# Kernel optimization log

Measured on AMD Instinct MI355X. Metric: run time of the kernel, lower is better.

The kernel has to match this reference:

```python
import jax, jax.numpy as jnp
import numpy as np


def _rope(xh, theta_factor):
    # xh: [H, S, Dqk]; rotate first half against second half (as in source)
    S, D = xh.shape[-2], xh.shape[-1]
    d_rope = D // 2
    rate = theta_factor * (-jnp.arange(0, d_rope, dtype=xh.dtype) / d_rope)
    pos = jnp.arange(0, S, dtype=xh.dtype)
    rot = pos[:, None] * rate[None, :]            # [S, d_rope]
    sin, cos = jnp.sin(rot), jnp.cos(rot)
    x1, x2 = xh[..., :d_rope], xh[..., d_rope:]
    y1 = cos * x1 - sin * x2
    y2 = sin * x1 + cos * x2
    return jnp.concatenate([y1, y2], axis=-1)


def _mha(x, y, q, k, v, o, theta_factor):
    S = x.shape[0]
    d_model = x.shape[1]
    x_scale = 1.0 / jnp.sqrt(jnp.array(x.shape[1], x.dtype))
    y_scale = 1.0 / jnp.sqrt(jnp.array(y.shape[1], x.dtype))
    # causal additive mask: 0 on/below diagonal, -1e9 above
    mask = (jnp.tril(jnp.ones((S, S), x.dtype)) - 1.0) * 1000000000.0
    # per-head projections (note: source uses x_scale for both q and k)
    pre_q = jnp.einsum('sd,hdk->hsk', x, q) * x_scale
    pre_k = jnp.einsum('td,hdk->htk', y, k) * x_scale
    vs = jnp.einsum('td,hdv->htv', y, v) * y_scale
    rq = _rope(pre_q, theta_factor)
    rk = _rope(pre_k, theta_factor)
    attn_scale = 1.0 / jnp.sqrt(jnp.array(rq.shape[-1], x.dtype))
    scores = jnp.einsum('hsk,htk->hst', rq, rk) * attn_scale + mask
    w = jax.nn.softmax(scores, axis=-1)           # [H, S, S]
    z = jnp.einsum('hst,htv->hsv', w, vs)         # [H, S, Dv]
    out_scale = 1.0 / jnp.sqrt(jnp.array(o.shape[0] * o.shape[1], x.dtype))
    return jnp.einsum('hsv,hvd->sd', z, o) * out_scale


def setup_inputs() -> dict:
    key = jax.random.key(0)
    ks = jax.random.split(key, 5)
    S, D, H, Dqk, Dv = 2048, 2048, 16, 128, 128
    return {
        'x': jax.random.normal(ks[0], (S, D), jnp.float32),
        'q': jax.random.normal(ks[1], (H, D, Dqk), jnp.float32),
        'k': jax.random.normal(ks[2], (H, D, Dqk), jnp.float32),
        'v': jax.random.normal(ks[3], (H, D, Dv), jnp.float32),
        'o': jax.random.normal(ks[4], (H, Dv, D), jnp.float32),
        'theta_factor': jnp.array(10000.0, jnp.float32),
    }


def reference(x, q, k, v, o, theta_factor):
    # self-attention path (y = x), scale = 1
    return _mha(x, x, q, k, v, o, theta_factor)
```

## Files before the change

### kernel.cpp

```cpp
#include <hip/hip_runtime.h>


#define S_LEN   2048
#define D_MODEL 2048
#define NHEAD   16
#define DHEAD   128

using f32x4   = __attribute__((ext_vector_type(4))) float;
using f32x16  = __attribute__((ext_vector_type(16))) float;
using bf16x8  = __attribute__((ext_vector_type(8))) __bf16;

__device__ __forceinline__ unsigned short f2bf(float f) {
  unsigned int u = __builtin_bit_cast(unsigned int, f);
  u += 0x7fffu + ((u >> 16) & 1u);
  return (unsigned short)(u >> 16);
}
__device__ __forceinline__ int chunks_of(int qt) { return (4 * qt + 13) / 10; }

__device__ __forceinline__ void gl_lds16(const unsigned short* g, char* l) {
  __builtin_amdgcn_global_load_lds(
      (const __attribute__((address_space(1))) unsigned int*)g,
      (__attribute__((address_space(3))) unsigned int*)l, 16, 0, 0);
}

__global__ void k_cvt(const float* __restrict__ in, unsigned short* __restrict__ out) {
  int i = (blockIdx.x * 256 + threadIdx.x) * 4;
  float4 v = *reinterpret_cast<const float4*>(in + i);
  ushort4 o; o.x = f2bf(v.x); o.y = f2bf(v.y); o.z = f2bf(v.z); o.w = f2bf(v.w);
  *reinterpret_cast<ushort4*>(out + i) = o;
}

__global__ void k_tab(const float* __restrict__ theta_p, float* __restrict__ sint,
                      float* __restrict__ cost) {
  int i = blockIdx.x * 256 + threadIdx.x;
  int s = i >> 6, c = i & 63;
  float rate = theta_p[0] * (-(float)c / 64.0f);
  float sn, cs;
  sincosf((float)s * rate, &sn, &cs);
  sint[i] = sn; cost[i] = cs;
}

__global__ void k_tr(const float* __restrict__ in, unsigned short* __restrict__ out,
                     int R, int C) {
  __shared__ float t[32][33];
  int b = blockIdx.x, rt = blockIdx.y, ct = blockIdx.z;
  const float* ip = in + (size_t)b * R * C;
  unsigned short* op = out + (size_t)b * R * C;
  int tx = threadIdx.x & 31, ty = threadIdx.x >> 5;
  #pragma unroll
  for (int i = 0; i < 4; i++)
    t[ty + i * 8][tx] = ip[(size_t)(rt * 32 + ty + i * 8) * C + ct * 32 + tx];
  __syncthreads();
  #pragma unroll
  for (int i = 0; i < 4; i++)
    op[(size_t)(ct * 32 + ty + i * 8) * R + rt * 32 + tx] = f2bf(t[tx][ty + i * 8]);
}

__global__ __launch_bounds__(256) void k_proj2(
    const unsigned short* __restrict__ xb, const unsigned short* __restrict__ wT,
    const float* __restrict__ sint, const float* __restrict__ cost,
    unsigned short* __restrict__ rq, unsigned short* __restrict__ rk,
    unsigned short* __restrict__ vst) {
  __shared__ char lds[65536];
  const int tid = threadIdx.x, l = tid & 63, w = tid >> 6;
  const int lr = l & 15, lk = l >> 4;
  const int orig = blockIdx.x;
  const int wg = (orig & 7) * 96 + (orig >> 3);
  const int bx = wg & 15, by = wg >> 4;
  const int s0 = bx * 128;
  const int h = by & 15, which = by >> 4;
  const unsigned short* bbase = wT + (size_t)by * 128 * D_MODEL;

  f32x4 acc[2][8] = {};

  auto stage = [&](int t, int buf) {
    const int kt = t * 64;
    char* dst = lds + buf * 32768;
    #pragma unroll
    for (int j = 0; j < 4; j++) {
      int ci = (j * 4 + w) * 64 + l;
      int r = ci >> 3, c8 = ci & 7;
      int csrc = (c8 ^ (r & 7)) * 8;
      gl_lds16(xb + (size_t)(s0 + r) * D_MODEL + kt + csrc, dst + ci * 16);
      gl_lds16(bbase + (size_t)r * D_MODEL + kt + csrc, dst + 16384 + ci * 16);
    }
  };

  stage(0, 0);
  int cur = 0;
  const int nT = D_MODEL / 64;
  for (int t = 0; t < nT; t++) {
    if (t + 1 < nT) {
      stage(t + 1, cur ^ 1);
      asm volatile("s_waitcnt vmcnt(8)" ::: "memory");
    } else {
      asm volatile("s_waitcnt vmcnt(0)" ::: "memory");
    }
    __builtin_amdgcn_s_barrier();
    const char* base = lds + cur * 32768;
    #pragma unroll
    for (int kk = 0; kk < 2; kk++) {
      const int kb = kk * 64 + lk * 16;
      bf16x8 a[2], b[8];
      #pragma unroll
      for (int mf = 0; mf < 2; mf++) {
        int rr = w * 32 + mf * 16 + lr;
        a[mf] = *reinterpret_cast<const bf16x8*>(base + rr * 128 + (kb ^ ((rr & 7) << 4)));
      }
      #pragma unroll
      for (int nf = 0; nf < 8; nf++) {
        int rn = nf * 16 + lr;
        b[nf] = *reinterpret_cast<const bf16x8*>(base + 16384 + rn * 128 + (kb ^ ((rn & 7) << 4)));
      }
      #pragma unroll
      for (int mf = 0; mf < 2; mf++)
        #pragma unroll
        for (int nf = 0; nf < 8; nf++)
          acc[mf][nf] = __builtin_amdgcn_mfma_f32_16x16x32_bf16(a[mf], b[nf], acc[mf][nf], 0, 0, 0);
    }
    asm volatile("s_waitcnt lgkmcnt(0)" ::: "memory");
    __builtin_amdgcn_s_barrier();
    cur ^= 1;
  }

  const float xscale = 0.022097086912079608f;
  const float qsc = xscale * 0.08838834764831845f;
  if (which < 2) {
    const float sc_out = (which == 0) ? qsc : xscale;
    unsigned short* dst = (which == 0 ? rq : rk) + (size_t)h * S_LEN * DHEAD;
    #pragma unroll
    for (int mf = 0; mf < 2; mf++) {
      #pragma unroll
      for (int nf = 0; nf < 4; nf++) {
        int c1 = nf * 16 + lr;
        #pragma unroll
        for (int rg = 0; rg < 4; rg++) {
          int srow = s0 + w * 32 + mf * 16 + lk * 4 + rg;
          float sn = sint[srow * 64 + c1], cs = cost[srow * 64 + c1];
          float x1 = acc[mf][nf][rg] * sc_out;
          float x2 = acc[mf][nf + 4][rg] * sc_out;
          dst[(size_t)srow * DHEAD + c1]      = f2bf(cs * x1 - sn * x2);
          dst[(size_t)srow * DHEAD + c1 + 64] = f2bf(sn * x1 + cs * x2);
        }
      }
    }
  } else {
    unsigned short* dst = vst + (size_t)h * DHEAD * S_LEN;
    #pragma unroll
    for (int mf = 0; mf < 2; mf++) {
      int rbase = s0 + w * 32 + mf * 16 + lk * 4;
      #pragma unroll
      for (int nf = 0; nf < 8; nf++) {
        int c = nf * 16 + lr;
        ushort4 ov;
        ov.x = f2bf(acc[mf][nf][0] * xscale); ov.y = f2bf(acc[mf][nf][1] * xscale);
        ov.z = f2bf(acc[mf][nf][2] * xscale); ov.w = f2bf(acc[mf][nf][3] * xscale);
        *reinterpret_cast<ushort4*>(dst + (size_t)c * S_LEN + rbase) = ov;
      }
    }
  }
}

__global__ __launch_bounds__(256, 2) void k_attn5(
    const unsigned short* __restrict__ rq, const unsigned short* __restrict__ rk,
    const unsigned short* __restrict__ vst,
    unsigned short* __restrict__ opart, float2* __restrict__ mlbuf) {
  __shared__ uint4 ldsbuf[1184];
  char* lds = (char*)ldsbuf;
  const int tid = threadIdx.x, l = tid & 63, w = tid >> 6;
  const int hi = l >> 5, qcol = l & 31;
  const int b = blockIdx.x;
  const int h = b & 15;
  int u = b >> 4, qt = 0;
  while (u >= chunks_of(qt)) { u -= chunks_of(qt); qt++; }
  const int ntile = 4 * qt + 4;
  const int tbeg = u * 10;
  const int tend = (tbeg + 10 < ntile) ? tbeg + 10 : ntile;
  const int s0w = qt * 128 + w * 32;
  const int wlast = s0w + 31;
  const int dtile = s0w >> 5;

  const unsigned short* rk_h  = rk  + (size_t)h * S_LEN * DHEAD;
  const unsigned short* vst_h = vst + (size_t)h * DHEAD * S_LEN;

  const unsigned short* qrow_p = rq + ((size_t)h * S_LEN + s0w + qcol) * DHEAD + hi * 8;
  bf16x8 qb[8];
  #pragma unroll
  for (int kk = 0; kk < 8; kk++)
    qb[kk] = *reinterpret_cast<const bf16x8*>(qrow_p + kk * 16);

  f32x16 O[4] = {};
  float mrow = -3.0e38f, lrow = 0.0f;

  uint4 kreg[2], vreg[2];
  {
    const int t0 = tbeg * 32;
    #pragma unroll
    for (int j = 0; j < 2; j++) {
      int ci = tid + j * 256;
      kreg[j] = *reinterpret_cast<const uint4*>(rk_h + (size_t)(t0 + (ci >> 4)) * DHEAD + (ci & 15) * 8);
      vreg[j] = *reinterpret_cast<const uint4*>(vst_h + (size_t)(ci >> 2) * S_LEN + t0 + (ci & 3) * 8);
    }
  }

  for (int t = tbeg; t < tend; t++) {
    __syncthreads();
    #pragma unroll
    for (int j = 0; j < 2; j++) {
      int ci = tid + j * 256;
      *reinterpret_cast<uint4*>(lds + (ci >> 4) * 272 + (ci & 15) * 16) = kreg[j];
      *reinterpret_cast<uint4*>(lds + 8704 + (ci >> 2) * 80 + (ci & 3) * 16) = vreg[j];
    }
    if (t + 1 < tend) {
      const int t0n = (t + 1) * 32;
      #pragma unroll
      for (int j = 0; j < 2; j++) {
        int ci = tid + j * 256;
        kreg[j] = *reinterpret_cast<const uint4*>(rk_h + (size_t)(t0n + (ci >> 4)) * DHEAD + (ci & 15) * 8);
        vreg[j] = *reinterpret_cast<const uint4*>(vst_h + (size_t)(ci >> 2) * S_LEN + t0n + (ci & 3) * 8);
      }
    }
    __syncthreads();
    const int tt0 = t * 32;
    if (tt0 <= wlast) {
      f32x16 sc = {};
      #pragma unroll
      for (int kk = 0; kk < 8; kk++) {
        bf16x8 ka = *reinterpret_cast<const bf16x8*>(lds + qcol * 272 + kk * 32 + hi * 16);
        sc = __builtin_amdgcn_mfma_f32_32x32x16_bf16(ka, qb[kk], sc, 0, 0, 0);
      }
      float p[16];
      #pragma unroll
      for (int r = 0; r < 16; r++) p[r] = sc[r];
      if (t == dtile) {
        #pragma unroll
        for (int r = 0; r < 16; r++)
          if (((r & 3) + 8 * (r >> 2) + 4 * hi) > qcol) p[r] = -1.0e9f;
      }
      float mx[8];
      #pragma unroll
      for (int i = 0; i < 8; i++) mx[i] = fmaxf(p[2 * i], p[2 * i + 1]);
      #pragma unroll
      for (int i = 0; i < 4; i++) mx[i] = fmaxf(mx[i], mx[i + 4]);
      mx[0] = fmaxf(mx[0], mx[2]); mx[1] = fmaxf(mx[1], mx[3]);
      float pmax = fmaxf(mx[0], mx[1]);
      pmax = fmaxf(pmax, __shfl_xor(pmax, 32, 64));
      if (__any(pmax > mrow + 8.0f)) {
        float mn = fmaxf(mrow, pmax);
        float sf = __expf(mrow - mn);
        lrow *= sf; mrow = mn;
        #pragma unroll
        for (int vc = 0; vc < 4; vc++)
          #pragma unroll
          for (int r = 0; r < 16; r++) O[vc][r] *= sf;
      }
      #pragma unroll
      for (int r = 0; r < 16; r++) p[r] = __expf(p[r] - mrow);
      float sm[8];
      #pragma unroll
      for (int i = 0; i < 8; i++) sm[i] = p[2 * i] + p[2 * i + 1];
      #pragma unroll
      for (int i = 0; i < 4; i++) sm[i] += sm[i + 4];
      float psum = (sm[0] + sm[1]) + (sm[2] + sm[3]);
      psum += __shfl_xor(psum, 32, 64);
      lrow += psum;
      unsigned int pk[2][4], sw[2][4];
      #pragma unroll
      for (int c = 0; c < 2; c++)
        #pragma unroll
        for (int k = 0; k < 4; k++) {
          unsigned int r_;
          asm("v_cvt_pk_bf16_f32 %0, %1, %2" : "=v"(r_)
              : "v"(p[8 * c + 2 * k]), "v"(p[8 * c + 2 * k + 1]));
          pk[c][k] = r_;
          sw[c][k] = (unsigned int)__shfl_xor((int)r_, 32, 64);
        }
      bf16x8 pb[2];
      #pragma unroll
      for (int c = 0; c < 2; c++) {
        union { unsigned int u4[4]; bf16x8 v; } bw;
        bw.u4[0] = hi ? sw[c][2] : pk[c][0];
        bw.u4[1] = hi ? sw[c][3] : pk[c][1];
        bw.u4[2] = hi ? pk[c][2] : sw[c][0];
        bw.u4[3] = hi ? pk[c][3] : sw[c][1];
        pb[c] = bw.v;
      }
      #pragma unroll
      for (int vc = 0; vc < 4; vc++) {
        const char* vrow = lds + 8704 + (vc * 32 + qcol) * 80 + hi * 16;
        bf16x8 va0 = *reinterpret_cast<const bf16x8*>(vrow);
        bf16x8 va1 = *reinterpret_cast<const bf16x8*>(vrow + 32);
        O[vc] = __builtin_amdgcn_mfma_f32_32x32x16_bf16(va0, pb[0], O[vc], 0, 0, 0);
        O[vc] = __builtin_amdgcn_mfma_f32_32x32x16_bf16(va1, pb[1], O[vc], 0, 0, 0);
      }
    }
  }
  float inv = lrow > 0.0f ? 1.0f / lrow : 0.0f;
  unsigned short* op = opart + ((size_t)b * 128 + w * 32 + qcol) * DHEAD;
  #pragma unroll
  for (int vc = 0; vc < 4; vc++)
    #pragma unroll
    for (int g = 0; g < 4; g++) {
      int v0 = vc * 32 + 8 * g + 4 * hi;
      ushort4 ov;
      ov.x = f2bf(O[vc][4 * g + 0] * inv); ov.y = f2bf(O[vc][4 * g + 1] * inv);
      ov.z = f2bf(O[vc][4 * g + 2] * inv); ov.w = f2bf(O[vc][4 * g + 3] * inv);
      *reinterpret_cast<ushort4*>(op + v0) = ov;
    }
  if (l < 32)
    mlbuf[(size_t)b * 128 + w * 32 + l] = make_float2(mrow, lrow);
}

__global__ void k_comb2(const unsigned short* __restrict__ opart,
                        const float2* __restrict__ mlbuf,
                        unsigned short* __restrict__ z) {
  int g = blockIdx.x * 256 + threadIdx.x;
  int vg = g & 15, q = (g >> 4) & 2047, h = g >> 15;
  int qt = q >> 7, r = q & 127;
  int base = 0;
  for (int j = 0; j < qt; j++) base += chunks_of(j);
  const int nc = chunks_of(qt);
  float m = -3.0e38f;
  float2 ml[7];
  #pragma unroll
  for (int cc = 0; cc < 7; cc++)
    if (cc < nc) {
      ml[cc] = mlbuf[(size_t)((base + cc) * 16 + h) * 128 + r];
      m = fmaxf(m, ml[cc].x);
    }
  float wts[7], wsum = 0.0f;
  #pragma unroll
  for (int cc = 0; cc < 7; cc++)
    if (cc < nc) {
      float wv = ml[cc].y > 0.0f ? ml[cc].y * __expf(ml[cc].x - m) : 0.0f;
      wts[cc] = wv; wsum += wv;
    }
  float wi = 1.0f / wsum;
  float acc[8] = {};
  #pragma unroll
  for (int cc = 0; cc < 7; cc++)
    if (cc < nc && wts[cc] > 0.0f) {
      float wv = wts[cc] * wi;
      bf16x8 v = *reinterpret_cast<const bf16x8*>(
          opart + ((size_t)((base + cc) * 16 + h) * 128 + r) * DHEAD + vg * 8);
      #pragma unroll
      for (int j = 0; j < 8; j++) acc[j] += wv * (float)v[j];
    }
  unsigned short* zp = z + (size_t)q * D_MODEL + h * DHEAD + vg * 8;
  ushort4 lo, hi4;
  lo.x = f2bf(acc[0]); lo.y = f2bf(acc[1]); lo.z = f2bf(acc[2]); lo.w = f2bf(acc[3]);
  hi4.x = f2bf(acc[4]); hi4.y = f2bf(acc[5]); hi4.z = f2bf(acc[6]); hi4.w = f2bf(acc[7]);
  *reinterpret_cast<ushort4*>(zp) = lo;
  *reinterpret_cast<ushort4*>(zp + 4) = hi4;
}

__global__ __launch_bounds__(256) void k_out2(
    const unsigned short* __restrict__ zb, const unsigned short* __restrict__ obT,
    float* __restrict__ out) {
  __shared__ char lds[65536];
  const int tid = threadIdx.x, l = tid & 63, w = tid >> 6;
  const int lr = l & 15, lk = l >> 4;
  const int orig = blockIdx.x;
  const int wg = (orig & 7) * 32 + (orig >> 3);
  const int bx = wg & 15, by = wg >> 4;
  const int s0 = bx * 128, n0 = by * 128;
  const int wm = w >> 1, wn = w & 1;
  f32x4 acc[4][4] = {};

  auto stage = [&](int t, int buf) {
    const int kt = t * 64;
    char* dst = lds + buf * 32768;
    #pragma unroll
    for (int j = 0; j < 4; j++) {
      int ci = (j * 4 + w) * 64 + l;
      int r = ci >> 3, c8 = ci & 7;
      int csrc = (c8 ^ (r & 7)) * 8;
      gl_lds16(zb + (size_t)(s0 + r) * D_MODEL + kt + csrc, dst + ci * 16);
      gl_lds16(obT + (size_t)(n0 + r) * D_MODEL + kt + csrc, dst + 16384 + ci * 16);
    }
  };

  stage(0, 0);
  int cur = 0;
  const int nT = D_MODEL / 64;
  for (int t = 0; t < nT; t++) {
    if (t + 1 < nT) {
      stage(t + 1, cur ^ 1);
      asm volatile("s_waitcnt vmcnt(8)" ::: "memory");
    } else {
      asm volatile("s_waitcnt vmcnt(0)" ::: "memory");
    }
    __builtin_amdgcn_s_barrier();
    const char* base = lds + cur * 32768;
    #pragma unroll
    for (int kk = 0; kk < 2; kk++) {
      const int kb = kk * 64 + lk * 16;
      bf16x8 a[4], b[4];
      #pragma unroll
      for (int mf = 0; mf < 4; mf++) {
        int rr = wm * 64 + mf * 16 + lr;
        a[mf] = *reinterpret_cast<const bf16x8*>(base + rr * 128 + (kb ^ ((rr & 7) << 4)));
      }
      #pragma unroll
      for (int nf = 0; nf < 4; nf++) {
        int rn = wn * 64 + nf * 16 + lr;
        b[nf] = *reinterpret_cast<const bf16x8*>(base + 16384 + rn * 128 + (kb ^ ((rn & 7) << 4)));
      }
      #pragma unroll
      for (int mf = 0; mf < 4; mf++)
        #pragma unroll
        for (int nf = 0; nf < 4; nf++)
          acc[mf][nf] = __builtin_amdgcn_mfma_f32_16x16x32_bf16(a[mf], b[nf], acc[mf][nf], 0, 0, 0);
    }
    asm volatile("s_waitcnt lgkmcnt(0)" ::: "memory");
    __builtin_amdgcn_s_barrier();
    cur ^= 1;
  }
  const float osc = 0.022097086912079608f;
  #pragma unroll
  for (int mf = 0; mf < 4; mf++)
    #pragma unroll
    for (int nf = 0; nf < 4; nf++)
      #pragma unroll
      for (int rg = 0; rg < 4; rg++)
        out[(size_t)(s0 + wm * 64 + mf * 16 + lk * 4 + rg) * D_MODEL + n0 + wn * 64 + nf * 16 + lr]
            = acc[mf][nf][rg] * osc;
}

extern "C" void kernel_launch(void* const* d_in, const int* in_sizes, int n_in,
                              void* d_out, int out_size, void* d_ws, size_t ws_size,
                              hipStream_t stream) {
  const float* x = (const float*)d_in[0];
  const float* q = (const float*)d_in[1];
  const float* k = (const float*)d_in[2];
  const float* v = (const float*)d_in[3];
  const float* o = (const float*)d_in[4];
  const float* theta = (const float*)d_in[5];
  float* out = (float*)d_out;

  char* ws = (char*)d_ws;
  const size_t MB = 1u << 20;
  unsigned short* xb  = (unsigned short*)(ws + 0 * MB);
  unsigned short* qbT = (unsigned short*)(ws + 8 * MB);
  unsigned short* kbT = (unsigned short*)(ws + 16 * MB);
  unsigned short* vbT = (unsigned short*)(ws + 24 * MB);
  unsigned short* obT = (unsigned short*)(ws + 32 * MB);
  unsigned short* rq  = (unsigned short*)(ws + 40 * MB);
  unsigned short* rk  = (unsigned short*)(ws + 48 * MB);
  unsigned short* vst = (unsigned short*)(ws + 56 * MB);
  float* sint = (float*)(ws + 64 * MB);
  float* cost = (float*)(ws + 64 * MB + 512 * 1024);
  unsigned short* opart = (unsigned short*)(ws + 0 * MB);
  float2* mlbuf         = (float2*)(ws + 31 * MB);
  unsigned short* zb    = (unsigned short*)(ws + 40 * MB);

  k_cvt<<<dim3(4096), dim3(256), 0, stream>>>(x, xb);
  k_tab<<<dim3(512), dim3(256), 0, stream>>>(theta, sint, cost);
  k_tr<<<dim3(16, 64, 4), dim3(256), 0, stream>>>(q, qbT, 2048, 128);
  k_tr<<<dim3(16, 64, 4), dim3(256), 0, stream>>>(k, kbT, 2048, 128);
  k_tr<<<dim3(16, 64, 4), dim3(256), 0, stream>>>(v, vbT, 2048, 128);
  k_tr<<<dim3(1, 64, 64), dim3(256), 0, stream>>>(o, obT, 2048, 2048);
  k_proj2<<<dim3(768), dim3(256), 0, stream>>>(xb, qbT, sint, cost, rq, rk, vst);
  k_attn5<<<dim3(976), dim3(256), 0, stream>>>(rq, rk, vst, opart, mlbuf);
  k_comb2<<<dim3(2048), dim3(256), 0, stream>>>(opart, mlbuf, zb);
  k_out2<<<dim3(256), dim3(256), 0, stream>>>(zb, obT, out);
}
```

Measured before the change: 200.5 us.

## Double-buffer K/V tiles in LDS and stage output through LDS for coalesced stores

```diff
diff --git a/kernel.cpp b/kernel.cpp
--- a/kernel.cpp
+++ b/kernel.cpp
@@ -161,11 +161,11 @@
   }
 }
 
-__global__ __launch_bounds__(256, 2) void k_attn5(
+__global__ __launch_bounds__(256, 2) void k_attn6(
     const unsigned short* __restrict__ rq, const unsigned short* __restrict__ rk,
     const unsigned short* __restrict__ vst,
     unsigned short* __restrict__ opart, float2* __restrict__ mlbuf) {
-  __shared__ uint4 ldsbuf[1184];
+  __shared__ uint4 ldsbuf[2368];
   char* lds = (char*)ldsbuf;
   const int tid = threadIdx.x, l = tid & 63, w = tid >> 6;
   const int hi = l >> 5, qcol = l & 31;
@@ -193,40 +193,41 @@
   float mrow = -3.0e38f, lrow = 0.0f;
 
   uint4 kreg[2], vreg[2];
-  {
-    const int t0 = tbeg * 32;
+  auto ld_regs = [&](int t) {
+    const int t0 = t * 32;
     #pragma unroll
     for (int j = 0; j < 2; j++) {
       int ci = tid + j * 256;
       kreg[j] = *reinterpret_cast<const uint4*>(rk_h + (size_t)(t0 + (ci >> 4)) * DHEAD + (ci & 15) * 8);
       vreg[j] = *reinterpret_cast<const uint4*>(vst_h + (size_t)(ci >> 2) * S_LEN + t0 + (ci & 3) * 8);
     }
-  }
-
-  for (int t = tbeg; t < tend; t++) {
-    __syncthreads();
+  };
+  auto wr_lds = [&](int p) {
+    char* dst = lds + p * 18944;
     #pragma unroll
     for (int j = 0; j < 2; j++) {
       int ci = tid + j * 256;
-      *reinterpret_cast<uint4*>(lds + (ci >> 4) * 272 + (ci & 15) * 16) = kreg[j];
-      *reinterpret_cast<uint4*>(lds + 8704 + (ci >> 2) * 80 + (ci & 3) * 16) = vreg[j];
-    }
-    if (t + 1 < tend) {
-      const int t0n = (t + 1) * 32;
-      #pragma unroll
-      for (int j = 0; j < 2; j++) {
-        int ci = tid + j * 256;
-        kreg[j] = *reinterpret_cast<const uint4*>(rk_h + (size_t)(t0n + (ci >> 4)) * DHEAD + (ci & 15) * 8);
-        vreg[j] = *reinterpret_cast<const uint4*>(vst_h + (size_t)(ci >> 2) * S_LEN + t0n + (ci & 3) * 8);
-      }
-    }
-    __syncthreads();
+      *reinterpret_cast<uint4*>(dst + (ci >> 4) * 272 + (ci & 15) * 16) = kreg[j];
+      *reinterpret_cast<uint4*>(dst + 8704 + (ci >> 2) * 80 + (ci & 3) * 16) = vreg[j];
+    }
+  };
+
+  ld_regs(tbeg);
+  wr_lds(0);
+  if (tbeg + 1 < tend) ld_regs(tbeg + 1);
+  asm volatile("s_waitcnt lgkmcnt(0)" ::: "memory");
+  __builtin_amdgcn_s_barrier();
+
+  int cur = 0;
+  for (int t = tbeg; t < tend; t++) {
+    const char* kb = lds + cur * 18944;
+    const char* vb = kb + 8704;
     const int tt0 = t * 32;
     if (tt0 <= wlast) {
       f32x16 sc = {};
       #pragma unroll
       for (int kk = 0; kk < 8; kk++) {
-        bf16x8 ka = *reinterpret_cast<const bf16x8*>(lds + qcol * 272 + kk * 32 + hi * 16);
+        bf16x8 ka = *reinterpret_cast<const bf16x8*>(kb + qcol * 272 + kk * 32 + hi * 16);
         sc = __builtin_amdgcn_mfma_f32_32x32x16_bf16(ka, qb[kk], sc, 0, 0, 0);
       }
       float p[16];
@@ -287,16 +288,24 @@
       }
       #pragma unroll
       for (int vc = 0; vc < 4; vc++) {
-        const char* vrow = lds + 8704 + (vc * 32 + qcol) * 80 + hi * 16;
+        const char* vrow = vb + (vc * 32 + qcol) * 80 + hi * 16;
         bf16x8 va0 = *reinterpret_cast<const bf16x8*>(vrow);
         bf16x8 va1 = *reinterpret_cast<const bf16x8*>(vrow + 32);
         O[vc] = __builtin_amdgcn_mfma_f32_32x32x16_bf16(va0, pb[0], O[vc], 0, 0, 0);
         O[vc] = __builtin_amdgcn_mfma_f32_32x32x16_bf16(va1, pb[1], O[vc], 0, 0, 0);
       }
     }
+    if (t + 1 < tend) {
+      wr_lds(cur ^ 1);
+      if (t + 2 < tend) ld_regs(t + 2);
+    }
+    asm volatile("s_waitcnt lgkmcnt(0)" ::: "memory");
+    __builtin_amdgcn_s_barrier();
+    cur ^= 1;
   }
+
+  __syncthreads();
   float inv = lrow > 0.0f ? 1.0f / lrow : 0.0f;
-  unsigned short* op = opart + ((size_t)b * 128 + w * 32 + qcol) * DHEAD;
   #pragma unroll
   for (int vc = 0; vc < 4; vc++)
     #pragma unroll
@@ -305,8 +314,15 @@
       ushort4 ov;
       ov.x = f2bf(O[vc][4 * g + 0] * inv); ov.y = f2bf(O[vc][4 * g + 1] * inv);
       ov.z = f2bf(O[vc][4 * g + 2] * inv); ov.w = f2bf(O[vc][4 * g + 3] * inv);
-      *reinterpret_cast<ushort4*>(op + v0) = ov;
-    }
+      *reinterpret_cast<ushort4*>(lds + (w * 32 + qcol) * 272 + v0 * 2) = ov;
+    }
+  __syncthreads();
+  #pragma unroll
+  for (int j = 0; j < 8; j++) {
+    int row = w * 32 + j * 4 + (l >> 4);
+    uint4 vv = *reinterpret_cast<const uint4*>(lds + row * 272 + (l & 15) * 16);
+    *reinterpret_cast<uint4*>(opart + ((size_t)b * 128 + row) * DHEAD + (l & 15) * 8) = vv;
+  }
   if (l < 32)
     mlbuf[(size_t)b * 128 + w * 32 + l] = make_float2(mrow, lrow);
 }
@@ -461,7 +477,7 @@
   k_tr<<<dim3(16, 64, 4), dim3(256), 0, stream>>>(v, vbT, 2048, 128);
   k_tr<<<dim3(1, 64, 64), dim3(256), 0, stream>>>(o, obT, 2048, 2048);
   k_proj2<<<dim3(768), dim3(256), 0, stream>>>(xb, qbT, sint, cost, rq, rk, vst);
-  k_attn5<<<dim3(976), dim3(256), 0, stream>>>(rq, rk, vst, opart, mlbuf);
+  k_attn6<<<dim3(976), dim3(256), 0, stream>>>(rq, rk, vst, opart, mlbuf);
   k_comb2<<<dim3(2048), dim3(256), 0, stream>>>(opart, mlbuf, zb);
   k_out2<<<dim3(256), dim3(256), 0, stream>>>(zb, obT, out);
 }
```

Result: faster. 192.1 us (-4.2%).
